# Kernel tuning notes

Measured on AMD Instinct MI355X. Metric: run time of the kernel, lower is better.

Reference implementation:

```python
import jax, jax.numpy as jnp
import numpy as np

L = 2048           # lattice side
R = 2.777          # public-goods multiplier r
GAMMA = 0.8
ETA = 0.8
K_FERMI = 0.5      # fermi temperature used in fermiUpdate


def _plus_sum(x):
    """3x3 plus-kernel conv with circular (wrap) padding == self + 4 rolled neighbors."""
    return (x
            + jnp.roll(x, 1, 0) + jnp.roll(x, -1, 0)
            + jnp.roll(x, 1, 1) + jnp.roll(x, -1, 1))


def setup_inputs() -> dict:
    key = jax.random.key(0)
    k1, k2, k3, k4, k5 = jax.random.split(key, 5)
    return {
        "type_t_minus": jax.random.randint(k1, (L, L), 0, 2, dtype=jnp.int32),
        "type_t": jax.random.randint(k2, (L, L), 0, 2, dtype=jnp.int32),
        "Q_tensor": jax.random.normal(k3, (L * L, 2, 2), dtype=jnp.float32),
        "learning_direction": jax.random.randint(k4, (L, L), 0, 4, dtype=jnp.int32),
        "learning_probabilities": jax.random.uniform(k5, (L, L), dtype=jnp.float32),
    }


def reference(type_t_minus, type_t, Q_tensor, learning_direction, learning_probabilities):
    N = L * L
    # ---- calculation_value: per-cell payoff from the 5 overlapping PGG games ----
    c = (type_t == 1).astype(jnp.float32)   # cooperator mask
    d = (type_t == 0).astype(jnp.float32)   # defector mask
    coop_num = _plus_sum(c)                  # cooperators in own 5-cell group
    base = coop_num * (R / 5.0)
    profit = _plus_sum(base - 1.0) * c + _plus_sum(base) * d   # [L, L]

    # ---- updateQMatrix: Q[C, A, B] <- (1-eta)*Q[C,A,B] + eta*(profit + gamma*max_b Q[C,B,b]) ----
    A = type_t_minus.reshape(-1)             # previous action, [N]
    B = type_t.reshape(-1)                   # current action,  [N]
    Qb = jnp.take_along_axis(Q_tensor, B[:, None, None], axis=1)[:, 0, :]  # Q[C, B, :] -> [N, 2]
    max_values = Qb.max(axis=1)              # [N]
    flatQ = Q_tensor.reshape(N, 4)
    idx = A * 2 + B                          # flattened (A, B) index
    old = jnp.take_along_axis(flatQ, idx[:, None], axis=1)[:, 0]
    upd = (1.0 - ETA) * old + ETA * (profit.reshape(-1) + GAMMA * max_values)
    Q_new = flatQ.at[jnp.arange(N), idx].set(upd).reshape(N, 2, 2)

    # ---- fermiUpdate: gather just-updated Q[C,A,B] (== upd), compare with 4 neighbors ----
    pm = upd.reshape(L, L)                   # fermi profit matrix

    def W(shift, axis):
        return 1.0 / (1.0 + jnp.exp((pm - jnp.roll(pm, shift, axis)) / K_FERMI))

    Ws = jnp.stack([W(1, 1), W(-1, 1), W(1, 0), W(-1, 0)])        # left,right,up,down [4,L,L]
    nb = jnp.stack([jnp.roll(type_t, 1, 1), jnp.roll(type_t, -1, 1),
                    jnp.roll(type_t, 1, 0), jnp.roll(type_t, -1, 0)])
    W_sel = jnp.take_along_axis(Ws, learning_direction[None], axis=0)[0]
    nb_sel = jnp.take_along_axis(nb, learning_direction[None], axis=0)[0]
    type_t1 = jnp.where(learning_probabilities <= W_sel, nb_sel, type_t)  # [L, L] int32

    return (Q_new, type_t1, profit)
```

## Files before the change

### kernel.cpp

```cpp
#include <hip/hip_runtime.h>


#define LSIDE 2048
#define LMASK 2047
#define LSHIFT 11
#define NCELL (LSIDE * LSIDE)

#define TROWS 7
#define TCOLS 264

__global__ __launch_bounds__(256) void spgg_fused(
    const int* __restrict__ tmin,
    const int* __restrict__ tt,
    const float* __restrict__ Q,
    const int* __restrict__ ldir,
    const float* __restrict__ lp,
    float* __restrict__ Qn,
    float* __restrict__ prof,
    float* __restrict__ t1out)
{
    __shared__ int tile[TROWS][TCOLS];

    const int t   = threadIdx.x;
    const int blk = blockIdx.x;
    const int i   = blk >> 3;
    const int j0  = (blk & 7) << 8;

    for (int k = t; k < TROWS * (TCOLS / 4); k += 256) {
        int r = k / (TCOLS / 4);
        int m = k - r * (TCOLS / 4);
        int row_g = (i + r - 3) & LMASK;
        int col_g = (j0 - 4 + (m << 2)) & LMASK;
        int4 v = *(const int4*)&tt[(row_g << LSHIFT) + col_g];
        *(int4*)&tile[r][m << 2] = v;
    }
    __syncthreads();

    const float KB        = 0.5554f;
    const float ETA       = 0.8f;
    const float ONE_M_ETA = 0.2f;
    const float GAMMA     = 0.8f;

#define M(r, c) (tile[r][c] == 1)

    auto profit_at = [&](int r, int c) -> float {
        int m_cc = M(r, c);
        int cn_c = m_cc + M(r-1, c) + M(r+1, c) + M(r, c-1) + M(r, c+1);
        int cn_u = M(r-1, c) + M(r-2, c) + m_cc + M(r-1, c-1) + M(r-1, c+1);
        int cn_d = M(r+1, c) + m_cc + M(r+2, c) + M(r+1, c-1) + M(r+1, c+1);
        int cn_l = M(r, c-1) + M(r-1, c-1) + M(r+1, c-1) + M(r, c-2) + m_cc;
        int cn_r = M(r, c+1) + M(r-1, c+1) + M(r+1, c+1) + m_cc + M(r, c+2);
        float b_c = __fmul_rn((float)cn_c, KB);
        float b_u = __fmul_rn((float)cn_u, KB);
        float b_d = __fmul_rn((float)cn_d, KB);
        float b_l = __fmul_rn((float)cn_l, KB);
        float b_r = __fmul_rn((float)cn_r, KB);
        float s0 = __fadd_rn(__fadd_rn(__fadd_rn(__fadd_rn(b_c, b_u), b_d), b_l), b_r);
        float s1 = __fadd_rn(__fadd_rn(__fadd_rn(__fadd_rn(
                       __fsub_rn(b_c, 1.0f), __fsub_rn(b_u, 1.0f)),
                       __fsub_rn(b_d, 1.0f)), __fsub_rn(b_l, 1.0f)),
                       __fsub_rn(b_r, 1.0f));
        return m_cc ? s1 : s0;
    };

    auto upd_of = [&](float profit, float4 qr, int A, int B) -> float {
        float q0 = (B == 0) ? qr.x : qr.z;
        float q1 = (B == 0) ? qr.y : qr.w;
        float mx = fmaxf(q0, q1);
        int k = A * 2 + B;
        float old = (k == 0) ? qr.x : ((k == 1) ? qr.y : ((k == 2) ? qr.z : qr.w));
        float t0 = __fmul_rn(GAMMA, mx);
        float t1 = __fadd_rn(profit, t0);
        float t2 = __fmul_rn(ETA, t1);
        float t3 = __fmul_rn(ONE_M_ETA, old);
        return __fadd_rn(t3, t2);
    };

    const int j   = j0 + t;
    const int idx = (i << LSHIFT) + j;
    const int lr  = 3, lc = t + 4;

    float p_own = profit_at(lr, lc);
    float4 qr   = ((const float4*)Q)[idx];
    int B = tile[lr][lc];
    int A = tmin[idx];
    float upd = upd_of(p_own, qr, A, B);

    int k = A * 2 + B;
    float4 qo;
    qo.x = (k == 0) ? upd : qr.x;
    qo.y = (k == 1) ? upd : qr.y;
    qo.z = (k == 2) ? upd : qr.z;
    qo.w = (k == 3) ? upd : qr.w;
    ((float4*)Qn)[idx] = qo;
    prof[idx] = p_own;

    int dir = ldir[idx];
    int di = (dir == 3) - (dir == 2);
    int dj = (dir == 1) - (dir == 0);
    int ni = (i + di) & LMASK;
    int nj = (j + dj) & LMASK;
    int nidx = (ni << LSHIFT) + nj;

    float p_nb  = profit_at(lr + di, lc + dj);
    float4 qn4  = ((const float4*)Q)[nidx];
    int Bn = tile[lr + di][lc + dj];
    int An = tmin[nidx];
    float upd_nb = upd_of(p_nb, qn4, An, Bn);

    float e1 = __fsub_rn(upd, upd_nb);
    float e2 = __fmul_rn(e1, 2.0f);
    float ex = (float)exp((double)e2);
    float W  = __fdiv_rn(1.0f, __fadd_rn(1.0f, ex));
    float pv = lp[idx];
    int sel = (pv <= W) ? Bn : B;
    t1out[idx] = (float)sel;
#undef M
}

extern "C" void kernel_launch(void* const* d_in, const int* in_sizes, int n_in,
                              void* d_out, int out_size, void* d_ws, size_t ws_size,
                              hipStream_t stream) {
    const int*   type_t_minus = (const int*)d_in[0];
    const int*   type_t       = (const int*)d_in[1];
    const float* Q_tensor     = (const float*)d_in[2];
    const int*   ldir         = (const int*)d_in[3];
    const float* lprob        = (const float*)d_in[4];

    float* out   = (float*)d_out;
    float* Qn    = out;
    float* t1out = out + (size_t)4 * NCELL;
    float* prof  = out + (size_t)5 * NCELL;

    const int threads = 256;
    const int blocks  = NCELL / threads;
    spgg_fused<<<blocks, threads, 0, stream>>>(type_t_minus, type_t, Q_tensor,
                                               ldir, lprob, Qn, prof, t1out);
}
```

Baseline: 216.5 us.

## Use per-wavefront shared tiles without block barrier and hoist global loads

Each 64-lane wavefront now stages its own 7x72 halo tile of type_t, so the block-wide __syncthreads is removed and waves proceed independently. All per-cell and neighbor global loads (Q, tmin, ldir, lp) are issued up front, before the profit computation, so their latency overlaps with the tile fill. The cost is more redundant halo reads: each 64-column wave loads 8 extra columns instead of 8 per 256. It also relies on intra-wavefront lockstep for LDS visibility without an explicit barrier.

```diff
diff --git a/kernel.cpp b/kernel.cpp
--- a/kernel.cpp
+++ b/kernel.cpp
@@ -5,9 +5,6 @@
 #define LMASK 2047
 #define LSHIFT 11
 #define NCELL (LSIDE * LSIDE)
-
-#define TROWS 7
-#define TCOLS 264
 
 __global__ __launch_bounds__(256) void spgg_fused(
     const int* __restrict__ tmin,
@@ -19,29 +16,53 @@
     float* __restrict__ prof,
     float* __restrict__ t1out)
 {
-    __shared__ int tile[TROWS][TCOLS];
+    __shared__ int tile[4][7][72];
 
-    const int t   = threadIdx.x;
-    const int blk = blockIdx.x;
-    const int i   = blk >> 3;
-    const int j0  = (blk & 7) << 8;
+    const int tid = threadIdx.x;
+    const int w   = tid >> 6;
+    const int l   = tid & 63;
+    const int idx = blockIdx.x * 256 + tid;
+    const int i   = idx >> LSHIFT;
+    const int j   = idx & LMASK;
+    const int j0w = j & ~63;
 
-    for (int k = t; k < TROWS * (TCOLS / 4); k += 256) {
-        int r = k / (TCOLS / 4);
-        int m = k - r * (TCOLS / 4);
-        int row_g = (i + r - 3) & LMASK;
-        int col_g = (j0 - 4 + (m << 2)) & LMASK;
-        int4 v = *(const int4*)&tt[(row_g << LSHIFT) + col_g];
-        *(int4*)&tile[r][m << 2] = v;
+    {
+        const int base_row = i - 3;
+        const int base_col = j0w - 4;
+#pragma unroll
+        for (int p = 0; p < 2; ++p) {
+            int k = l + (p << 6);
+            if (k < 126) {
+                int r = (k * 57) >> 10;
+                int m = k - r * 18;
+                int rg = (base_row + r) & LMASK;
+                int cg = (base_col + (m << 2)) & LMASK;
+                int4 v = *(const int4*)&tt[(rg << LSHIFT) + cg];
+                *(int4*)&tile[w][r][m << 2] = v;
+            }
+        }
     }
-    __syncthreads();
+
+    float4 qr = ((const float4*)Q)[idx];
+    int    A  = tmin[idx];
+    int    dir = ldir[idx];
+    float  pv  = lp[idx];
+
+    int di = (dir == 3) - (dir == 2);
+    int dj = (dir == 1) - (dir == 0);
+    int ni = (i + di) & LMASK;
+    int nj = (j + dj) & LMASK;
+    int nidx = (ni << LSHIFT) + nj;
+
+    float4 qn4 = ((const float4*)Q)[nidx];
+    int    An  = tmin[nidx];
 
     const float KB        = 0.5554f;
     const float ETA       = 0.8f;
     const float ONE_M_ETA = 0.2f;
     const float GAMMA     = 0.8f;
 
-#define M(r, c) (tile[r][c] == 1)
+#define M(r, c) (tile[w][r][c] == 1)
 
     auto profit_at = [&](int r, int c) -> float {
         int m_cc = M(r, c);
@@ -63,12 +84,12 @@
         return m_cc ? s1 : s0;
     };
 
-    auto upd_of = [&](float profit, float4 qr, int A, int B) -> float {
-        float q0 = (B == 0) ? qr.x : qr.z;
-        float q1 = (B == 0) ? qr.y : qr.w;
+    auto upd_of = [&](float profit, float4 q4, int Ax, int Bx) -> float {
+        float q0 = (Bx == 0) ? q4.x : q4.z;
+        float q1 = (Bx == 0) ? q4.y : q4.w;
         float mx = fmaxf(q0, q1);
-        int k = A * 2 + B;
-        float old = (k == 0) ? qr.x : ((k == 1) ? qr.y : ((k == 2) ? qr.z : qr.w));
+        int k = Ax * 2 + Bx;
+        float old = (k == 0) ? q4.x : ((k == 1) ? q4.y : ((k == 2) ? q4.z : q4.w));
         float t0 = __fmul_rn(GAMMA, mx);
         float t1 = __fadd_rn(profit, t0);
         float t2 = __fmul_rn(ETA, t1);
@@ -76,14 +97,10 @@
         return __fadd_rn(t3, t2);
     };
 
-    const int j   = j0 + t;
-    const int idx = (i << LSHIFT) + j;
-    const int lr  = 3, lc = t + 4;
+    const int lr = 3, lc = l + 4;
 
     float p_own = profit_at(lr, lc);
-    float4 qr   = ((const float4*)Q)[idx];
-    int B = tile[lr][lc];
-    int A = tmin[idx];
+    int B = tile[w][lr][lc];
     float upd = upd_of(p_own, qr, A, B);
 
     int k = A * 2 + B;
@@ -95,24 +112,14 @@
     ((float4*)Qn)[idx] = qo;
     prof[idx] = p_own;
 
-    int dir = ldir[idx];
-    int di = (dir == 3) - (dir == 2);
-    int dj = (dir == 1) - (dir == 0);
-    int ni = (i + di) & LMASK;
-    int nj = (j + dj) & LMASK;
-    int nidx = (ni << LSHIFT) + nj;
-
-    float p_nb  = profit_at(lr + di, lc + dj);
-    float4 qn4  = ((const float4*)Q)[nidx];
-    int Bn = tile[lr + di][lc + dj];
-    int An = tmin[nidx];
+    float p_nb = profit_at(lr + di, lc + dj);
+    int Bn = tile[w][lr + di][lc + dj];
     float upd_nb = upd_of(p_nb, qn4, An, Bn);
 
     float e1 = __fsub_rn(upd, upd_nb);
     float e2 = __fmul_rn(e1, 2.0f);
     float ex = (float)exp((double)e2);
     float W  = __fdiv_rn(1.0f, __fadd_rn(1.0f, ex));
-    float pv = lp[idx];
     int sel = (pv <= W) ? Bn : B;
     t1out[idx] = (float)sel;
 #undef M
```

Measured after the change: 218.3 us. About the same (+0.9%).
